# Optimization experiments

Hardware: AMD Instinct MI355X
Metric: run time of the kernel (lower is better)

## Reference

```python
import jax, jax.numpy as jnp
import numpy as np

N_EMBED = 288
HEAD_SIZE = 32


def setup_inputs() -> dict:
    key = jax.random.key(0)
    kx, kk, kq, kv = jax.random.split(key, 4)
    B, T, C = 16, 2048, N_EMBED
    scale = 1.0 / np.sqrt(C)
    return {
        "x": jax.random.normal(kx, (B, T, C), dtype=jnp.float32),
        # Linear(n_embed, head_size, bias=False) weights, stored as [C, head_size]
        "Wk": jax.random.normal(kk, (C, HEAD_SIZE), dtype=jnp.float32) * scale,
        "Wq": jax.random.normal(kq, (C, HEAD_SIZE), dtype=jnp.float32) * scale,
        "Wv": jax.random.normal(kv, (C, HEAD_SIZE), dtype=jnp.float32) * scale,
    }


def reference(x, Wk, Wq, Wv):
    # x: [B, T, C]
    k = x @ Wk  # [B, T, hs]
    q = x @ Wq
    v = x @ Wv
    # NOTE: source computes k @ q^T (not q @ k^T) -- reproduce faithfully.
    weights = jnp.einsum("bth,bsh->bts", k, q) * (HEAD_SIZE ** -0.5)  # [B, T, T]
    T = x.shape[1]
    causal = jnp.tril(jnp.ones((T, T), dtype=bool))
    weights = jnp.where(causal, weights, -jnp.inf)
    weights = jax.nn.softmax(weights, axis=-1)
    return weights @ v  # [B, T, hs]
```

## Files before the change

kernel.cpp:

```cpp
#include <hip/hip_runtime.h>

typedef __bf16 bf16;
typedef __attribute__((ext_vector_type(8))) __bf16 bf16x8;
typedef __attribute__((ext_vector_type(4))) __bf16 bf16x4;
typedef __attribute__((ext_vector_type(4))) short s16x4;
typedef __attribute__((ext_vector_type(4))) float f32x4;

#define BATCH 16
#define SEQ   2048
#define CEMB  288
#define HS    32
#define NROWS (BATCH * SEQ)

#if __has_builtin(__builtin_amdgcn_mfma_f32_16x16x16bf16_1k)
#define HAVE_MFMA16 1
#define MFMA16(a, b, c) __builtin_amdgcn_mfma_f32_16x16x16bf16_1k((a), (b), (c), 0, 0, 0)
#else
#define HAVE_MFMA16 0
#endif

#define XSTR 296

__global__ __launch_bounds__(384) void proj_kernel(
    const float* __restrict__ x, const float* __restrict__ Wk,
    const float* __restrict__ Wq, const float* __restrict__ Wv,
    bf16* __restrict__ Kx, bf16* __restrict__ Qm, bf16* __restrict__ VT)
{
    __shared__ __align__(16) bf16 Xl[32 * XSTR];

    const int tid  = threadIdx.x;
    const int wv   = tid >> 6;
    const int lane = tid & 63;
    const int quad = lane >> 4;
    const int ln   = lane & 15;
    const int dsel = wv >> 1;
    const int half = wv & 1;

    const float SCALE = 0.25519486439582695f;

    const float* Wsrc = (dsel == 0) ? Wk : ((dsel == 1) ? Wq : Wv);
    const float mul = (dsel == 0) ? SCALE : 1.0f;
    bf16x8 wfrag[9];
    for (int kc = 0; kc < 9; ++kc) {
        bf16x8 f;
#pragma unroll
        for (int j = 0; j < 8; ++j) {
            float w = Wsrc[(kc * 32 + quad * 8 + j) * HS + half * 16 + ln];
            f[j] = (bf16)(w * mul);
        }
        wfrag[kc] = f;
    }

    const int wgRowBase = blockIdx.x * 64;
    for (int it = 0; it < 2; ++it) {
        __syncthreads();
        const int rb = wgRowBase + it * 32;
#pragma unroll
        for (int i = 0; i < 6; ++i) {
            int f = tid + 384 * i;
            int row = f / 72;
            int c4  = f - row * 72;
            f32x4 v = ((const f32x4*)x)[(rb + row) * 72 + c4];
            bf16* d = &Xl[row * XSTR + c4 * 4];
            d[0] = (bf16)v[0]; d[1] = (bf16)v[1];
            d[2] = (bf16)v[2]; d[3] = (bf16)v[3];
        }
        __syncthreads();

#pragma unroll
        for (int m = 0; m < 2; ++m) {
            f32x4 acc = {0.f, 0.f, 0.f, 0.f};
#pragma unroll
            for (int kc = 0; kc < 9; ++kc) {
                bf16x8 a = *(const bf16x8*)&Xl[(m * 16 + ln) * XSTR + kc * 32 + quad * 8];
                acc = __builtin_amdgcn_mfma_f32_16x16x32_bf16(a, wfrag[kc], acc, 0, 0, 0);
            }
#pragma unroll
            for (int reg = 0; reg < 4; ++reg) {
                int gr = rb + m * 16 + quad * 4 + reg;
                bf16 val = (bf16)acc[reg];
                if (dsel == 0) {
                    Kx[gr * HS + half * 16 + ln] = val;
                } else if (dsel == 1) {
                    Qm[gr * HS + half * 16 + ln] = val;
                } else {
                    VT[(gr >> 11) * (HS * SEQ) + (half * 16 + ln) * SEQ + (gr & 2047)] = val;
                }
            }
        }
    }
}

#define PSTR 40

__global__ __launch_bounds__(256) void attn_kernel(
    const bf16* __restrict__ Kx, const bf16* __restrict__ Qm,
    const bf16* __restrict__ VT,
    float* __restrict__ Opart, float* __restrict__ Lpart)
{
#if !HAVE_MFMA16
    __shared__ __align__(16) bf16 Pl[4][16 * PSTR];
#endif

    const int tid  = threadIdx.x;
    const int w    = tid >> 6;
    const int lane = tid & 63;
    const int quad = lane >> 4;
    const int ln   = lane & 15;

    const int b = blockIdx.x & 15;
    const int j = (blockIdx.x >> 4) * 4 + w;
    int c, tt;
    if (j < 64)       { c = 0; tt = 63 - j; }
    else if (j < 112) { c = 1; tt = 63 - (j - 64); }
    else if (j < 144) { c = 2; tt = 63 - (j - 112); }
    else              { c = 3; tt = 63 - (j - 144); }

    const int tlo = tt * 32;
    const int cs  = c * 512;
    const int ce  = (cs + 512 < tlo + 32) ? (cs + 512) : (tlo + 32);

    const bf16* Kb = Kx + b * SEQ * HS;
    const bf16* Qb = Qm + b * SEQ * HS;
    const bf16* Vb = VT + b * HS * SEQ;

    bf16x8 kfragB[2];
#pragma unroll
    for (int th = 0; th < 2; ++th)
        kfragB[th] = *(const bf16x8*)&Kb[(tlo + th * 16 + ln) * HS + quad * 8];

    f32x4 Of[2][2] = {};
    f32x4 Lf[2]    = {};

#if HAVE_MFMA16
    s16x4 ones4;
#pragma unroll
    for (int i = 0; i < 4; ++i) ones4[i] = (short)0x3F80;

    bf16x8 qf[2];
    s16x4  vb[2][2];
    qf[0] = *(const bf16x8*)&Qb[(cs + ln) * HS + quad * 8];
    qf[1] = *(const bf16x8*)&Qb[(cs + 16 + ln) * HS + quad * 8];
#pragma unroll
    for (int sh = 0; sh < 2; ++sh)
#pragma unroll
        for (int hh = 0; hh < 2; ++hh)
            vb[sh][hh] = *(const s16x4*)&Vb[(hh * 16 + ln) * SEQ + cs + sh * 16 + quad * 4];

    for (int s0 = cs; s0 < ce; s0 += 32) {
        const int sn = (s0 + 32 < ce) ? (s0 + 32) : s0;
        bf16x8 qn0 = *(const bf16x8*)&Qb[(sn + ln) * HS + quad * 8];
        bf16x8 qn1 = *(const bf16x8*)&Qb[(sn + 16 + ln) * HS + quad * 8];
        s16x4  vn[2][2];
#pragma unroll
        for (int sh = 0; sh < 2; ++sh)
#pragma unroll
            for (int hh = 0; hh < 2; ++hh)
                vn[sh][hh] = *(const s16x4*)&Vb[(hh * 16 + ln) * SEQ + sn + sh * 16 + quad * 4];

#pragma unroll
        for (int th = 0; th < 2; ++th) {
            const int tbase = tlo + th * 16;
            if (s0 >= tbase + 16) continue;
            const int tcol = tbase + ln;
#pragma unroll
            for (int sh = 0; sh < 2; ++sh) {
                const int sb = s0 + sh * 16;
                if (sb >= tbase + 16) continue;
                const bool dmask = (sb == tbase);
                f32x4 z = {0.f, 0.f, 0.f, 0.f};
                f32x4 S = __builtin_amdgcn_mfma_f32_16x16x32_bf16(
                              qf[sh], kfragB[th], z, 0, 0, 0);
                const int sbase = sb + quad * 4;
                bf16x4 pk;
#pragma unroll
                for (int r = 0; r < 4; ++r) {
                    float p = __builtin_amdgcn_exp2f(S[r]);
                    if (dmask) p = (sbase + r <= tcol) ? p : 0.0f;
                    pk[r] = (bf16)p;
                }
                s16x4 ap = __builtin_bit_cast(s16x4, pk);
                Of[th][0] = MFMA16(ap, vb[sh][0], Of[th][0]);
                Of[th][1] = MFMA16(ap, vb[sh][1], Of[th][1]);
                Lf[th]    = MFMA16(ap, ones4,     Lf[th]);
            }
        }
        qf[0] = qn0; qf[1] = qn1;
#pragma unroll
        for (int sh = 0; sh < 2; ++sh)
#pragma unroll
            for (int hh = 0; hh < 2; ++hh)
                vb[sh][hh] = vn[sh][hh];
    }
#else
    bf16x8 ones;
#pragma unroll
    for (int i = 0; i < 8; ++i) ones[i] = (bf16)1.0f;
    bf16* P = &Pl[w][0];

    bf16x8 qf[2], vf[2];
    qf[0] = *(const bf16x8*)&Qb[(cs + ln) * HS + quad * 8];
    qf[1] = *(const bf16x8*)&Qb[(cs + 16 + ln) * HS + quad * 8];
    vf[0] = *(const bf16x8*)&Vb[ln * SEQ + cs + quad * 8];
    vf[1] = *(const bf16x8*)&Vb[(16 + ln) * SEQ + cs + quad * 8];

    for (int s0 = cs; s0 < ce; s0 += 32) {
        const int sn = (s0 + 32 < ce) ? (s0 + 32) : s0;
        bf16x8 qn0 = *(const bf16x8*)&Qb[(sn + ln) * HS + quad * 8];
        bf16x8 qn1 = *(const bf16x8*)&Qb[(sn + 16 + ln) * HS + quad * 8];
        bf16x8 vn0 = *(const bf16x8*)&Vb[ln * SEQ + sn + quad * 8];
        bf16x8 vn1 = *(const bf16x8*)&Vb[(16 + ln) * SEQ + sn + quad * 8];

#pragma unroll
        for (int th = 0; th < 2; ++th) {
            const int tbase = tlo + th * 16;
            if (s0 >= tbase + 16) continue;
            const bool diag = (s0 + 31 >= tbase);
            const int tcol = tbase + ln;
#pragma unroll
            for (int sh = 0; sh < 2; ++sh) {
                f32x4 z = {0.f, 0.f, 0.f, 0.f};
                f32x4 S = __builtin_amdgcn_mfma_f32_16x16x32_bf16(
                              qf[sh], kfragB[th], z, 0, 0, 0);
                const int sbase = s0 + sh * 16 + quad * 4;
                bf16x4 pk;
#pragma unroll
                for (int r = 0; r < 4; ++r) {
                    float p = __builtin_amdgcn_exp2f(S[r]);
                    if (diag) p = (sbase + r <= tcol) ? p : 0.0f;
                    pk[r] = (bf16)p;
                }
                *(bf16x4*)&P[ln * PSTR + sh * 16 + quad * 4] = pk;
            }
            asm volatile("" ::: "memory");
            bf16x8 ap = *(const bf16x8*)&P[ln * PSTR + quad * 8];
            asm volatile("" ::: "memory");
            Of[th][0] = __builtin_amdgcn_mfma_f32_16x16x32_bf16(ap, vf[0], Of[th][0], 0, 0, 0);
            Of[th][1] = __builtin_amdgcn_mfma_f32_16x16x32_bf16(ap, vf[1], Of[th][1], 0, 0, 0);
            Lf[th]    = __builtin_amdgcn_mfma_f32_16x16x32_bf16(ap, ones,  Lf[th],    0, 0, 0);
        }
        qf[0] = qn0; qf[1] = qn1; vf[0] = vn0; vf[1] = vn1;
    }
#endif

#pragma unroll
    for (int th = 0; th < 2; ++th) {
#pragma unroll
        for (int reg = 0; reg < 4; ++reg) {
            int gr = b * SEQ + tlo + th * 16 + quad * 4 + reg;
            float* od = Opart + ((size_t)c * NROWS + gr) * HS;
            od[ln]      = Of[th][0][reg];
            od[16 + ln] = Of[th][1][reg];
            if (ln == 0) Lpart[c * NROWS + gr] = Lf[th][reg];
        }
    }
}

__global__ __launch_bounds__(256) void combine_kernel(
    const float* __restrict__ Opart, const float* __restrict__ Lpart,
    float* __restrict__ out)
{
    int idx = blockIdx.x * 256 + threadIdx.x;
    int gr = idx >> 3, h4 = idx & 7;
    int t  = gr & 2047;
    int nc = (t >> 9) + 1;
    f32x4 acc = {0.f, 0.f, 0.f, 0.f};
    float l = 0.f;
    for (int c = 0; c < nc; ++c) {
        acc += ((const f32x4*)Opart)[((size_t)c * NROWS + gr) * 8 + h4];
        l   += Lpart[c * NROWS + gr];
    }
    f32x4 r = acc / l;
    ((f32x4*)out)[idx] = r;
}

extern "C" void kernel_launch(void* const* d_in, const int* in_sizes, int n_in,
                              void* d_out, int out_size, void* d_ws, size_t ws_size,
                              hipStream_t stream) {
    (void)in_sizes; (void)n_in; (void)out_size; (void)ws_size;
    const float* x  = (const float*)d_in[0];
    const float* Wk = (const float*)d_in[1];
    const float* Wq = (const float*)d_in[2];
    const float* Wv = (const float*)d_in[3];

    char* ws = (char*)d_ws;
    bf16*  Kx    = (bf16*)(ws);
    bf16*  Qm    = (bf16*)(ws + 2097152);
    bf16*  VT    = (bf16*)(ws + 4194304);
    float* Opart = (float*)(ws + 6291456);
    float* Lpart = (float*)(ws + 23068672);
    float* out   = (float*)d_out;

    hipLaunchKernelGGL(proj_kernel, dim3(512), dim3(384), 0, stream,
                       x, Wk, Wq, Wv, Kx, Qm, VT);
    hipLaunchKernelGGL(attn_kernel, dim3(640), dim3(256), 0, stream,
                       Kx, Qm, VT, Opart, Lpart);
    hipLaunchKernelGGL(combine_kernel, dim3(1024), dim3(256), 0, stream,
                       Opart, Lpart, out);
}
```

Measured before the change: 119.5 us.

## Split each query tile across four waves with LDS reduction, drop combine kernel

The attention kernel now gives each block one 32-row tile. Its four waves take interleaved 32-column key chunks, then reduce partial outputs and row sums through shared memory and write normalized results directly. This removes the separate combine kernel and the global Opart/Lpart round trip. The cost is a barrier plus LDS traffic per block, load imbalance across waves on short tiles, and blocks with only a few waves active near the start of the sequence.

```diff
diff --git a/kernel.cpp b/kernel.cpp
--- a/kernel.cpp
+++ b/kernel.cpp
@@ -12,11 +12,10 @@
 #define HS    32
 #define NROWS (BATCH * SEQ)
 
-#if __has_builtin(__builtin_amdgcn_mfma_f32_16x16x16bf16_1k)
-#define HAVE_MFMA16 1
+#if defined(__HIP_DEVICE_COMPILE__)
 #define MFMA16(a, b, c) __builtin_amdgcn_mfma_f32_16x16x16bf16_1k((a), (b), (c), 0, 0, 0)
 #else
-#define HAVE_MFMA16 0
+__device__ static inline f32x4 MFMA16(s16x4 a, s16x4 b, f32x4 c) { (void)a; (void)b; return c; }
 #endif
 
 #define XSTR 296
@@ -91,16 +90,12 @@
     }
 }
 
-#define PSTR 40
-
 __global__ __launch_bounds__(256) void attn_kernel(
     const bf16* __restrict__ Kx, const bf16* __restrict__ Qm,
-    const bf16* __restrict__ VT,
-    float* __restrict__ Opart, float* __restrict__ Lpart)
+    const bf16* __restrict__ VT, float* __restrict__ out)
 {
-#if !HAVE_MFMA16
-    __shared__ __align__(16) bf16 Pl[4][16 * PSTR];
-#endif
+    __shared__ f32x4 OlO[4][2][2][64];
+    __shared__ f32x4 Lred[4][2][64];
 
     const int tid  = threadIdx.x;
     const int w    = tid >> 6;
@@ -108,17 +103,10 @@
     const int quad = lane >> 4;
     const int ln   = lane & 15;
 
-    const int b = blockIdx.x & 15;
-    const int j = (blockIdx.x >> 4) * 4 + w;
-    int c, tt;
-    if (j < 64)       { c = 0; tt = 63 - j; }
-    else if (j < 112) { c = 1; tt = 63 - (j - 64); }
-    else if (j < 144) { c = 2; tt = 63 - (j - 112); }
-    else              { c = 3; tt = 63 - (j - 144); }
-
+    const int b   = blockIdx.x & 15;
+    const int tt  = 63 - (blockIdx.x >> 4);
     const int tlo = tt * 32;
-    const int cs  = c * 512;
-    const int ce  = (cs + 512 < tlo + 32) ? (cs + 512) : (tlo + 32);
+    const int send = tlo + 32;
 
     const bf16* Kb = Kx + b * SEQ * HS;
     const bf16* Qb = Qm + b * SEQ * HS;
@@ -129,149 +117,90 @@
     for (int th = 0; th < 2; ++th)
         kfragB[th] = *(const bf16x8*)&Kb[(tlo + th * 16 + ln) * HS + quad * 8];
 
+    s16x4 ones4;
+#pragma unroll
+    for (int i = 0; i < 4; ++i) ones4[i] = (short)0x3F80;
+
     f32x4 Of[2][2] = {};
     f32x4 Lf[2]    = {};
 
-#if HAVE_MFMA16
-    s16x4 ones4;
-#pragma unroll
-    for (int i = 0; i < 4; ++i) ones4[i] = (short)0x3F80;
-
-    bf16x8 qf[2];
-    s16x4  vb[2][2];
-    qf[0] = *(const bf16x8*)&Qb[(cs + ln) * HS + quad * 8];
-    qf[1] = *(const bf16x8*)&Qb[(cs + 16 + ln) * HS + quad * 8];
-#pragma unroll
-    for (int sh = 0; sh < 2; ++sh)
-#pragma unroll
-        for (int hh = 0; hh < 2; ++hh)
-            vb[sh][hh] = *(const s16x4*)&Vb[(hh * 16 + ln) * SEQ + cs + sh * 16 + quad * 4];
-
-    for (int s0 = cs; s0 < ce; s0 += 32) {
-        const int sn = (s0 + 32 < ce) ? (s0 + 32) : s0;
-        bf16x8 qn0 = *(const bf16x8*)&Qb[(sn + ln) * HS + quad * 8];
-        bf16x8 qn1 = *(const bf16x8*)&Qb[(sn + 16 + ln) * HS + quad * 8];
-        s16x4  vn[2][2];
+    int s0 = w * 32;
+    if (s0 < send) {
+        bf16x8 qf[2];
+        s16x4  vb[2][2];
+        qf[0] = *(const bf16x8*)&Qb[(s0 + ln) * HS + quad * 8];
+        qf[1] = *(const bf16x8*)&Qb[(s0 + 16 + ln) * HS + quad * 8];
 #pragma unroll
         for (int sh = 0; sh < 2; ++sh)
 #pragma unroll
             for (int hh = 0; hh < 2; ++hh)
-                vn[sh][hh] = *(const s16x4*)&Vb[(hh * 16 + ln) * SEQ + sn + sh * 16 + quad * 4];
-
-#pragma unroll
-        for (int th = 0; th < 2; ++th) {
-            const int tbase = tlo + th * 16;
-            if (s0 >= tbase + 16) continue;
-            const int tcol = tbase + ln;
-#pragma unroll
-            for (int sh = 0; sh < 2; ++sh) {
-                const int sb = s0 + sh * 16;
-                if (sb >= tbase + 16) continue;
-                const bool dmask = (sb == tbase);
-                f32x4 z = {0.f, 0.f, 0.f, 0.f};
-                f32x4 S = __builtin_amdgcn_mfma_f32_16x16x32_bf16(
-                              qf[sh], kfragB[th], z, 0, 0, 0);
-                const int sbase = sb + quad * 4;
-                bf16x4 pk;
-#pragma unroll
-                for (int r = 0; r < 4; ++r) {
-                    float p = __builtin_amdgcn_exp2f(S[r]);
-                    if (dmask) p = (sbase + r <= tcol) ? p : 0.0f;
-                    pk[r] = (bf16)p;
+                vb[sh][hh] = *(const s16x4*)&Vb[(hh * 16 + ln) * SEQ + s0 + sh * 16 + quad * 4];
+
+        for (; s0 < send; s0 += 128) {
+            const int sn = (s0 + 128 < send) ? (s0 + 128) : s0;
+            bf16x8 qn0 = *(const bf16x8*)&Qb[(sn + ln) * HS + quad * 8];
+            bf16x8 qn1 = *(const bf16x8*)&Qb[(sn + 16 + ln) * HS + quad * 8];
+            s16x4  vn[2][2];
+#pragma unroll
+            for (int sh = 0; sh < 2; ++sh)
+#pragma unroll
+                for (int hh = 0; hh < 2; ++hh)
+                    vn[sh][hh] = *(const s16x4*)&Vb[(hh * 16 + ln) * SEQ + sn + sh * 16 + quad * 4];
+
+#pragma unroll
+            for (int th = 0; th < 2; ++th) {
+                const int tbase = tlo + th * 16;
+                if (s0 >= tbase + 16) continue;
+                const int tcol = tbase + ln;
+#pragma unroll
+                for (int sh = 0; sh < 2; ++sh) {
+                    const int sb = s0 + sh * 16;
+                    if (sb >= tbase + 16) continue;
+                    const bool dmask = (sb == tbase);
+                    f32x4 z = {0.f, 0.f, 0.f, 0.f};
+                    f32x4 S = __builtin_amdgcn_mfma_f32_16x16x32_bf16(
+                                  qf[sh], kfragB[th], z, 0, 0, 0);
+                    const int sbase = sb + quad * 4;
+                    bf16x4 pk;
+#pragma unroll
+                    for (int r = 0; r < 4; ++r) {
+                        float p = __builtin_amdgcn_exp2f(S[r]);
+                        if (dmask) p = (sbase + r <= tcol) ? p : 0.0f;
+                        pk[r] = (bf16)p;
+                    }
+                    s16x4 ap = __builtin_bit_cast(s16x4, pk);
+                    Of[th][0] = MFMA16(ap, vb[sh][0], Of[th][0]);
+                    Of[th][1] = MFMA16(ap, vb[sh][1], Of[th][1]);
+                    Lf[th]    = MFMA16(ap, ones4,     Lf[th]);
                 }
-                s16x4 ap = __builtin_bit_cast(s16x4, pk);
-                Of[th][0] = MFMA16(ap, vb[sh][0], Of[th][0]);
-                Of[th][1] = MFMA16(ap, vb[sh][1], Of[th][1]);
-                Lf[th]    = MFMA16(ap, ones4,     Lf[th]);
             }
-        }
-        qf[0] = qn0; qf[1] = qn1;
-#pragma unroll
-        for (int sh = 0; sh < 2; ++sh)
-#pragma unroll
-            for (int hh = 0; hh < 2; ++hh)
-                vb[sh][hh] = vn[sh][hh];
-    }
-#else
-    bf16x8 ones;
-#pragma unroll
-    for (int i = 0; i < 8; ++i) ones[i] = (bf16)1.0f;
-    bf16* P = &Pl[w][0];
-
-    bf16x8 qf[2], vf[2];
-    qf[0] = *(const bf16x8*)&Qb[(cs + ln) * HS + quad * 8];
-    qf[1] = *(const bf16x8*)&Qb[(cs + 16 + ln) * HS + quad * 8];
-    vf[0] = *(const bf16x8*)&Vb[ln * SEQ + cs + quad * 8];
-    vf[1] = *(const bf16x8*)&Vb[(16 + ln) * SEQ + cs + quad * 8];
-
-    for (int s0 = cs; s0 < ce; s0 += 32) {
-        const int sn = (s0 + 32 < ce) ? (s0 + 32) : s0;
-        bf16x8 qn0 = *(const bf16x8*)&Qb[(sn + ln) * HS + quad * 8];
-        bf16x8 qn1 = *(const bf16x8*)&Qb[(sn + 16 + ln) * HS + quad * 8];
-        bf16x8 vn0 = *(const bf16x8*)&Vb[ln * SEQ + sn + quad * 8];
-        bf16x8 vn1 = *(const bf16x8*)&Vb[(16 + ln) * SEQ + sn + quad * 8];
-
-#pragma unroll
-        for (int th = 0; th < 2; ++th) {
-            const int tbase = tlo + th * 16;
-            if (s0 >= tbase + 16) continue;
-            const bool diag = (s0 + 31 >= tbase);
-            const int tcol = tbase + ln;
-#pragma unroll
-            for (int sh = 0; sh < 2; ++sh) {
-                f32x4 z = {0.f, 0.f, 0.f, 0.f};
-                f32x4 S = __builtin_amdgcn_mfma_f32_16x16x32_bf16(
-                              qf[sh], kfragB[th], z, 0, 0, 0);
-                const int sbase = s0 + sh * 16 + quad * 4;
-                bf16x4 pk;
-#pragma unroll
-                for (int r = 0; r < 4; ++r) {
-                    float p = __builtin_amdgcn_exp2f(S[r]);
-                    if (diag) p = (sbase + r <= tcol) ? p : 0.0f;
-                    pk[r] = (bf16)p;
-                }
-                *(bf16x4*)&P[ln * PSTR + sh * 16 + quad * 4] = pk;
-            }
-            asm volatile("" ::: "memory");
-            bf16x8 ap = *(const bf16x8*)&P[ln * PSTR + quad * 8];
-            asm volatile("" ::: "memory");
-            Of[th][0] = __builtin_amdgcn_mfma_f32_16x16x32_bf16(ap, vf[0], Of[th][0], 0, 0, 0);
-            Of[th][1] = __builtin_amdgcn_mfma_f32_16x16x32_bf16(ap, vf[1], Of[th][1], 0, 0, 0);
-            Lf[th]    = __builtin_amdgcn_mfma_f32_16x16x32_bf16(ap, ones,  Lf[th],    0, 0, 0);
-        }
-        qf[0] = qn0; qf[1] = qn1; vf[0] = vn0; vf[1] = vn1;
-    }
-#endif
+            qf[0] = qn0; qf[1] = qn1;
+#pragma unroll
+            for (int sh = 0; sh < 2; ++sh)
+#pragma unroll
+                for (int hh = 0; hh < 2; ++hh)
+                    vb[sh][hh] = vn[sh][hh];
+        }
+    }
 
 #pragma unroll
     for (int th = 0; th < 2; ++th) {
-#pragma unroll
-        for (int reg = 0; reg < 4; ++reg) {
-            int gr = b * SEQ + tlo + th * 16 + quad * 4 + reg;
-            float* od = Opart + ((size_t)c * NROWS + gr) * HS;
-            od[ln]      = Of[th][0][reg];
-            od[16 + ln] = Of[th][1][reg];
-            if (ln == 0) Lpart[c * NROWS + gr] = Lf[th][reg];
-        }
-    }
-}
-
-__global__ __launch_bounds__(256) void combine_kernel(
-    const float* __restrict__ Opart, const float* __restrict__ Lpart,
-    float* __restrict__ out)
-{
-    int idx = blockIdx.x * 256 + threadIdx.x;
-    int gr = idx >> 3, h4 = idx & 7;
-    int t  = gr & 2047;
-    int nc = (t >> 9) + 1;
-    f32x4 acc = {0.f, 0.f, 0.f, 0.f};
-    float l = 0.f;
-    for (int c = 0; c < nc; ++c) {
-        acc += ((const f32x4*)Opart)[((size_t)c * NROWS + gr) * 8 + h4];
-        l   += Lpart[c * NROWS + gr];
-    }
-    f32x4 r = acc / l;
-    ((f32x4*)out)[idx] = r;
+        OlO[w][th][0][lane] = Of[th][0];
+        OlO[w][th][1][lane] = Of[th][1];
+        Lred[w][th][lane]   = Lf[th];
+    }
+    __syncthreads();
+
+    const int fth = w >> 1, fhh = w & 1;
+    f32x4 o = OlO[0][fth][fhh][lane] + OlO[1][fth][fhh][lane]
+            + OlO[2][fth][fhh][lane] + OlO[3][fth][fhh][lane];
+    f32x4 l = Lred[0][fth][lane] + Lred[1][fth][lane]
+            + Lred[2][fth][lane] + Lred[3][fth][lane];
+#pragma unroll
+    for (int reg = 0; reg < 4; ++reg) {
+        int gr = b * SEQ + tlo + fth * 16 + quad * 4 + reg;
+        out[gr * HS + fhh * 16 + ln] = o[reg] / l[reg];
+    }
 }
 
 extern "C" void kernel_launch(void* const* d_in, const int* in_sizes, int n_in,
@@ -284,17 +213,13 @@
     const float* Wv = (const float*)d_in[3];
 
     char* ws = (char*)d_ws;
-    bf16*  Kx    = (bf16*)(ws);
-    bf16*  Qm    = (bf16*)(ws + 2097152);
-    bf16*  VT    = (bf16*)(ws + 4194304);
-    float* Opart = (float*)(ws + 6291456);
-    float* Lpart = (float*)(ws + 23068672);
-    float* out   = (float*)d_out;
+    bf16*  Kx = (bf16*)(ws);
+    bf16*  Qm = (bf16*)(ws + 2097152);
+    bf16*  VT = (bf16*)(ws + 4194304);
+    float* out = (float*)d_out;
 
     hipLaunchKernelGGL(proj_kernel, dim3(512), dim3(384), 0, stream,
                        x, Wk, Wq, Wv, Kx, Qm, VT);
-    hipLaunchKernelGGL(attn_kernel, dim3(640), dim3(256), 0, stream,
-                       Kx, Qm, VT, Opart, Lpart);
-    hipLaunchKernelGGL(combine_kernel, dim3(1024), dim3(256), 0, stream,
-                       Opart, Lpart, out);
+    hipLaunchKernelGGL(attn_kernel, dim3(1024), dim3(256), 0, stream,
+                       Kx, Qm, VT, out);
 }
```

New measurement: 112.4 us. 1.06x faster.
